# Performance work log

Measured on AMD Instinct MI355X. Metric: run time of the kernel, lower is better.

Reference implementation:

```python
import jax, jax.numpy as jnp
import numpy as np

K = 27  # num_neighs, hardcoded in module
EPS = 1e-5


def knn_idx(x, k):
    # x: (B, N, 3) -> (B, N, k) indices of k nearest neighbors (self included)
    xx = jnp.sum(x * x, axis=-1)                      # (B, N)
    inner = jnp.einsum('bnd,bmd->bnm', x, x)          # (B, N, N)
    d = 2.0 * inner - xx[:, :, None] - xx[:, None, :] # negative sq dist
    return jax.lax.top_k(d, k)[1]


def graph_feature(f, idx):
    # f: (B, N, C), idx: (B, N, k) -> (B, N, k, 2C) = [neigh - center, center]
    neigh = jax.vmap(lambda fb, ib: fb[ib])(f, idx)   # (B, N, k, C)
    center = jnp.broadcast_to(f[:, :, None, :], neigh.shape)
    return jnp.concatenate([neigh - center, center], axis=-1)


def bn_lrelu(y, g, b, axes):
    m = jnp.mean(y, axis=axes, keepdims=True)
    v = jnp.var(y, axis=axes, keepdims=True)
    y = (y - m) * jax.lax.rsqrt(v + EPS) * g + b
    return jnp.where(y >= 0, y, 0.2 * y)


def edge_conv(f, idx, W, g, b):
    # f: (B, N, C) -> (B, N, C_out); 1x1 conv over (B, 2C, N, k) + BN + LeakyReLU + max over k
    h = graph_feature(f, idx)                         # (B, N, k, 2C)
    y = jnp.einsum('bnkc,oc->bnko', h, W)             # (B, N, k, C_out)
    y = bn_lrelu(y, g, b, axes=(0, 1, 2))
    return jnp.max(y, axis=2)                         # (B, N, C_out)


def setup_inputs() -> dict:
    key = jax.random.key(0)
    ks = jax.random.split(key, 8)
    B, N, latent = 2, 2048, 256
    x = jax.random.normal(ks[0], (B, N, 3), dtype=jnp.float32)
    chans = [(6, 96), (192, 192), (384, 384), (768, 768)]
    inp = {'x': x}
    for i, (cin, cout) in enumerate(chans):
        inp[f'W{i}'] = jax.random.normal(ks[1 + i], (cout, cin), dtype=jnp.float32) * np.sqrt(2.0 / cin).astype(np.float32)
        inp[f'g{i}'] = jnp.ones((cout,), dtype=jnp.float32)
        inp[f'b{i}'] = jnp.zeros((cout,), dtype=jnp.float32)
    inp['W4'] = jax.random.normal(ks[5], (latent, 1440), dtype=jnp.float32) * np.sqrt(2.0 / 1440).astype(np.float32)
    inp['g4'] = jnp.ones((latent,), dtype=jnp.float32)
    inp['b4'] = jnp.zeros((latent,), dtype=jnp.float32)
    return inp


def reference(x, W0, g0, b0, W1, g1, b1, W2, g2, b2, W3, g3, b3, W4, g4, b4):
    # x: (B, N, 3)
    idx = knn_idx(x, K)                               # (B, N, K), fixed for all layers (only_true_neighs=True)
    outs = []
    f = x
    for (W, g, b) in ((W0, g0, b0), (W1, g1, b1), (W2, g2, b2), (W3, g3, b3)):
        f = edge_conv(f, idx, W, g, b)
        outs.append(f)
    h = jnp.concatenate(outs, axis=-1)                # (B, N, 1440)
    y = jnp.einsum('bnc,oc->bno', h, W4)              # (B, N, latent)
    feats = bn_lrelu(y, g4, b4, axes=(0, 1))          # features_per_point (B, N, latent)
    global_feat = jnp.max(feats, axis=1)              # (B, latent)
    return global_feat, feats
```

## Files before the change

### kernel.cpp

```cpp
#include <hip/hip_runtime.h>
#include <hip/hip_bf16.h>

#define BATCH 2
#define NPB   2048
#define NPTS  4096
#define KNB   27
#define FCATC 1440
#define CSTRIDE 1696
#define NSLOT 32
#define PBATCH 4

#define WOFF_L1 0
#define WOFF_L2 36864
#define WOFF_L3 184320
#define WOFF_F  774144
#define WTOTAL  1142784

typedef __hip_bfloat16 bf16;
typedef __attribute__((ext_vector_type(8))) short short8;
typedef __attribute__((ext_vector_type(4))) float f32x4;
typedef __attribute__((ext_vector_type(2))) short s16x2;

__device__ __forceinline__ float b2f(bf16 v) { return __bfloat162float(v); }

__device__ __forceinline__ void split_bf16(float v, bf16& h, bf16& l) {
    h = __float2bfloat16(v);
    l = __float2bfloat16(v - b2f(h));
}

__device__ __forceinline__ float ldin(const void* p, size_t i, int f32) {
    return f32 ? ((const float*)p)[i] : b2f(((const bf16*)p)[i]);
}

__global__ void k_init(const void* __restrict__ x, int* __restrict__ flag,
                       float* __restrict__ xf, float* __restrict__ slots) {
    if (blockIdx.x < 424) {
        slots[blockIdx.x * 256 + threadIdx.x] = 0.f;
        return;
    }
    __shared__ int s;
    if (threadIdx.x == 0) s = 0;
    __syncthreads();
    const bf16* xb = (const bf16*)x;
    int local = 0;
    for (int i = threadIdx.x; i < NPTS * 3; i += 256) {
        float v = b2f(xb[i]);
        if (!(fabsf(v) < 1e4f)) local = 1;
    }
    if (local) s = 1;
    __syncthreads();
    int f32 = s;
    if (threadIdx.x == 0) flag[0] = f32;
    for (int i = threadIdx.x; i < NPTS * 3; i += 256) xf[i] = ldin(x, i, f32);
}

__global__ __launch_bounds__(256) void k_knn(const float* __restrict__ x, int* __restrict__ idx) {
    __shared__ uint hist4[4][260];
    __shared__ uint hist[256];
    __shared__ int  tix[NPB];
    __shared__ uint s_phigh;
    __shared__ int  s_rem, s_outcnt, s_tiecnt;

    int bn = blockIdx.x, b = bn >> 11, n = bn & (NPB - 1);
    int tid = threadIdx.x;
    int wv = tid >> 6;
    const float* xb = x + (size_t)b * NPB * 3;
    float cx = xb[n * 3 + 0], cy = xb[n * 3 + 1], cz = xb[n * 3 + 2];
    float cc = cx * cx + cy * cy + cz * cz;

    uint u[8];
    #pragma unroll
    for (int j = 0; j < 8; j++) {
        int m = j * 256 + tid;
        float mx = xb[m * 3 + 0], my = xb[m * 3 + 1], mz = xb[m * 3 + 2];
        float d = 2.f * (cx * mx + cy * my + cz * mz) - cc - (mx * mx + my * my + mz * mz);
        uint s = __float_as_uint(d);
        u[j] = (s & 0x80000000u) ? ~s : (s | 0x80000000u);
    }
    if (tid == 0) { s_phigh = 0; s_rem = KNB; s_outcnt = 0; s_tiecnt = 0; }

    for (int pass = 0; pass < 4; pass++) {
        int shift = 24 - pass * 8;
        hist[tid] = 0;
        for (int i = tid; i < 4 * 260; i += 256) ((uint*)hist4)[i] = 0;
        __syncthreads();
        uint phigh = s_phigh;
        #pragma unroll
        for (int j = 0; j < 8; j++) {
            bool in = (pass == 0) || ((u[j] >> (shift + 8)) == phigh);
            if (in) atomicAdd(&hist4[wv][(u[j] >> shift) & 0xFFu], 1u);
        }
        __syncthreads();
        hist[tid] = hist4[0][tid] + hist4[1][tid] + hist4[2][tid] + hist4[3][tid];
        __syncthreads();
        if (tid < 64) {
            int L = tid;
            uint c0 = hist[L * 4 + 0], c1 = hist[L * 4 + 1], c2 = hist[L * 4 + 2], c3 = hist[L * 4 + 3];
            uint s = c0 + c1 + c2 + c3;
            uint acc = s;
            #pragma unroll
            for (int off = 1; off < 64; off <<= 1) {
                uint t = __shfl_down(acc, off);
                if (L + off < 64) acc += t;
            }
            uint excl = acc - s;
            int rem = s_rem;
            if ((int)excl < rem && (int)acc >= rem) {
                uint cs[4] = { c0, c1, c2, c3 };
                uint cum = excl;
                int bsel = 0; uint hb = 0;
                #pragma unroll
                for (int q = 3; q >= 0; q--) {
                    if ((int)cum < rem && (int)(cum + cs[q]) >= rem && hb == 0u && bsel == 0) {
                        bsel = L * 4 + q; hb = cs[q]; cum += cs[q];
                    } else if (bsel == 0 && hb == 0u) {
                        cum += cs[q];
                    }
                }
                int strictlyAbove = (int)(cum - hb);
                s_rem = rem - strictlyAbove;
                s_phigh = (phigh << 8) | (uint)bsel;
            }
        }
        __syncthreads();
    }

    uint T = s_phigh;
    #pragma unroll
    for (int j = 0; j < 8; j++) {
        int m = j * 256 + tid;
        if (u[j] > T) {
            int p = atomicAdd(&s_outcnt, 1);
            idx[bn * KNB + p] = b * NPB + m;
        } else if (u[j] == T) {
            int p = atomicAdd(&s_tiecnt, 1);
            tix[p] = m;
        }
    }
    __syncthreads();
    int outcnt = s_outcnt, rem = s_rem, tiecnt = s_tiecnt;
    if (tiecnt == rem) {
        if (tid < rem) idx[bn * KNB + outcnt + tid] = b * NPB + tix[tid];
    } else if (tid == 0) {
        for (int t = 0; t < rem; t++) {
            int bi = 0;
            for (int q = 1; q < tiecnt; q++) if (tix[q] < tix[bi]) bi = q;
            idx[bn * KNB + outcnt + t] = b * NPB + tix[bi];
            tix[bi] = 0x7fffffff;
        }
    }
}

__global__ void k_l0(const float* __restrict__ xf, const void* __restrict__ W,
                     const int* __restrict__ flag, bf16* __restrict__ Ub, float* __restrict__ Vf) {
    int i = blockIdx.x * 256 + threadIdx.x;
    if (i >= NPTS * 192) return;
    int bn = i / 192, o = i % 192;
    int f32 = flag[0];
    float x0 = xf[bn * 3 + 0], x1 = xf[bn * 3 + 1], x2 = xf[bn * 3 + 2];
    if (o < 96) {
        float r = x0 * ldin(W, o * 6 + 0, f32) + x1 * ldin(W, o * 6 + 1, f32) + x2 * ldin(W, o * 6 + 2, f32);
        Ub[(size_t)bn * 96 + o] = __float2bfloat16(r);
    } else {
        int oo = o - 96;
        float w0 = ldin(W, oo * 6 + 3, f32) - ldin(W, oo * 6 + 0, f32);
        float w1 = ldin(W, oo * 6 + 4, f32) - ldin(W, oo * 6 + 1, f32);
        float w2 = ldin(W, oo * 6 + 5, f32) - ldin(W, oo * 6 + 2, f32);
        Vf[(size_t)bn * 96 + oo] = x0 * w0 + x1 * w1 + x2 * w2;
    }
}

__global__ void k_wt_all(const void* __restrict__ W1, const void* __restrict__ W2,
                         const void* __restrict__ W3, const void* __restrict__ W4,
                         const int* __restrict__ flag,
                         bf16* __restrict__ Wh, bf16* __restrict__ Wl) {
    int i = blockIdx.x * 256 + threadIdx.x;
    if (i >= WTOTAL) return;
    int f32 = flag[0];
    float w;
    if (i < WOFF_L2) {
        int row = i / 96, c = i % 96;
        w = (row < 192) ? ldin(W1, (size_t)row * 192 + c, f32)
                        : ldin(W1, (size_t)(row - 192) * 192 + 96 + c, f32)
                          - ldin(W1, (size_t)(row - 192) * 192 + c, f32);
    } else if (i < WOFF_L3) {
        int j = i - WOFF_L2;
        int row = j / 192, c = j % 192;
        w = (row < 384) ? ldin(W2, (size_t)row * 384 + c, f32)
                        : ldin(W2, (size_t)(row - 384) * 384 + 192 + c, f32)
                          - ldin(W2, (size_t)(row - 384) * 384 + c, f32);
    } else if (i < WOFF_F) {
        int j = i - WOFF_L3;
        int row = j / 384, c = j % 384;
        w = (row < 768) ? ldin(W3, (size_t)row * 768 + c, f32)
                        : ldin(W3, (size_t)(row - 768) * 768 + 384 + c, f32)
                          - ldin(W3, (size_t)(row - 768) * 768 + c, f32);
    } else {
        int j = i - WOFF_F;
        w = ldin(W4, j, f32);
    }
    bf16 h, l; split_bf16(w, h, l);
    Wh[i] = h; Wl[i] = l;
}

__global__ __launch_bounds__(256) void k_gemm_mfma(const bf16* __restrict__ Ah, const bf16* __restrict__ Al,
                                                   int lda, int aoff,
                                                   const bf16* __restrict__ Bh, const bf16* __restrict__ Bl,
                                                   int K, bf16* __restrict__ Cu, float* __restrict__ Cv,
                                                   int Cosplit, int ldc, int ksz, int zstride) {
    __shared__ bf16 Ash[64][40];
    __shared__ bf16 Asl[64][40];
    __shared__ bf16 Bsh[64][40];
    __shared__ bf16 Bsl[64][40];
    int tid = threadIdx.x;
    int wave = tid >> 6, lane = tid & 63;
    int wm = wave >> 1, wn = wave & 1;
    int quad = lane >> 4, l15 = lane & 15;
    int Lxy = blockIdx.y * gridDim.x + blockIdx.x;
    int stripe = Lxy & 7;
    int w = Lxy >> 3;
    int mb = stripe * 8 + (w & 7);
    int nb = w >> 3;
    int m0 = mb * 64, n0 = nb * 64;
    int kbase = blockIdx.z * ksz;
    float* Cz = Cv + (size_t)blockIdx.z * zstride;
    int lr = tid >> 2, lc = (tid & 3) * 8;

    f32x4 acc[2][2] = {};
    for (int k0 = kbase; k0 < kbase + ksz; k0 += 32) {
        size_t ao = (size_t)(m0 + lr) * lda + aoff + k0 + lc;
        size_t bo = (size_t)(n0 + lr) * K + k0 + lc;
        *(short8*)&Ash[lr][lc] = *(const short8*)&Ah[ao];
        *(short8*)&Asl[lr][lc] = *(const short8*)&Al[ao];
        *(short8*)&Bsh[lr][lc] = *(const short8*)&Bh[bo];
        *(short8*)&Bsl[lr][lc] = *(const short8*)&Bl[bo];
        __syncthreads();
        short8 ah0 = *(const short8*)&Ash[wm * 32 + l15][quad * 8];
        short8 ah1 = *(const short8*)&Ash[wm * 32 + 16 + l15][quad * 8];
        short8 al0 = *(const short8*)&Asl[wm * 32 + l15][quad * 8];
        short8 al1 = *(const short8*)&Asl[wm * 32 + 16 + l15][quad * 8];
        short8 bh0 = *(const short8*)&Bsh[wn * 32 + l15][quad * 8];
        short8 bh1 = *(const short8*)&Bsh[wn * 32 + 16 + l15][quad * 8];
        short8 bl0 = *(const short8*)&Bsl[wn * 32 + l15][quad * 8];
        short8 bl1 = *(const short8*)&Bsl[wn * 32 + 16 + l15][quad * 8];
        acc[0][0] = __builtin_amdgcn_mfma_f32_16x16x32_bf16(ah0, bl0, acc[0][0], 0, 0, 0);
        acc[0][0] = __builtin_amdgcn_mfma_f32_16x16x32_bf16(al0, bh0, acc[0][0], 0, 0, 0);
        acc[0][0] = __builtin_amdgcn_mfma_f32_16x16x32_bf16(ah0, bh0, acc[0][0], 0, 0, 0);
        acc[0][1] = __builtin_amdgcn_mfma_f32_16x16x32_bf16(ah0, bl1, acc[0][1], 0, 0, 0);
        acc[0][1] = __builtin_amdgcn_mfma_f32_16x16x32_bf16(al0, bh1, acc[0][1], 0, 0, 0);
        acc[0][1] = __builtin_amdgcn_mfma_f32_16x16x32_bf16(ah0, bh1, acc[0][1], 0, 0, 0);
        acc[1][0] = __builtin_amdgcn_mfma_f32_16x16x32_bf16(ah1, bl0, acc[1][0], 0, 0, 0);
        acc[1][0] = __builtin_amdgcn_mfma_f32_16x16x32_bf16(al1, bh0, acc[1][0], 0, 0, 0);
        acc[1][0] = __builtin_amdgcn_mfma_f32_16x16x32_bf16(ah1, bh0, acc[1][0], 0, 0, 0);
        acc[1][1] = __builtin_amdgcn_mfma_f32_16x16x32_bf16(ah1, bl1, acc[1][1], 0, 0, 0);
        acc[1][1] = __builtin_amdgcn_mfma_f32_16x16x32_bf16(al1, bh1, acc[1][1], 0, 0, 0);
        acc[1][1] = __builtin_amdgcn_mfma_f32_16x16x32_bf16(ah1, bh1, acc[1][1], 0, 0, 0);
        __syncthreads();
    }
    #pragma unroll
    for (int mt = 0; mt < 2; mt++) {
        #pragma unroll
        for (int nt = 0; nt < 2; nt++) {
            int col = n0 + wn * 32 + nt * 16 + l15;
            #pragma unroll
            for (int i = 0; i < 4; i++) {
                int row = m0 + wm * 32 + mt * 16 + quad * 4 + i;
                if (Cosplit > 0) {
                    if (col < Cosplit) Cu[(size_t)row * Cosplit + col] = __float2bfloat16(acc[mt][nt][i]);
                    else               Cv[(size_t)row * Cosplit + col - Cosplit] = acc[mt][nt][i];
                } else {
                    Cz[(size_t)row * ldc + col] = acc[mt][nt][i];
                }
            }
        }
    }
}

__global__ __launch_bounds__(256) void k_gather(const bf16* __restrict__ Ub, float* __restrict__ Vf,
                                                const int* __restrict__ idx,
                                                bf16* __restrict__ fch, bf16* __restrict__ fcl,
                                                float* __restrict__ ssum, float* __restrict__ ssq,
                                                int Co, int out_off) {
    __shared__ int srow[PBATCH * KNB];
    int tid = threadIdx.x;
    int L = blockIdx.y * gridDim.x + blockIdx.x;
    int batch = L & 1;
    int w = L >> 1;
    int pg = batch * 512 + (w & 511);
    int chunk = w >> 9;
    int p0 = pg * PBATCH;
    if (tid < PBATCH * KNB) srow[tid] = idx[p0 * KNB + tid] * Co;
    __syncthreads();
    int P = Co >> 1;
    int op = chunk * 256 + tid;
    if (op >= P) return;
    int o = op * 2;
    int slot = pg & (NSLOT - 1);
    float s0 = 0.f, s1 = 0.f, q0 = 0.f, q1 = 0.f;
    #pragma unroll 1
    for (int p = 0; p < PBATCH; p++) {
        int bn = p0 + p;
        float2 vv = *(const float2*)&Vf[(size_t)bn * Co + o];
        float ymax0 = -INFINITY, ymax1 = -INFINITY, ymin0 = INFINITY, ymin1 = INFINITY;
        #pragma unroll
        for (int k = 0; k < KNB; k++) {
            uint wb = *(const uint*)&Ub[(size_t)srow[p * KNB + k] + o];
            float y0 = __uint_as_float(wb << 16) + vv.x;
            float y1 = __uint_as_float(wb & 0xffff0000u) + vv.y;
            ymax0 = fmaxf(ymax0, y0); ymin0 = fminf(ymin0, y0); s0 += y0; q0 += y0 * y0;
            ymax1 = fmaxf(ymax1, y1); ymin1 = fminf(ymin1, y1); s1 += y1; q1 += y1 * y1;
        }
        size_t fi = (size_t)bn * FCATC + out_off + o;
        bf16 hh[2], ll[2];
        split_bf16(ymax0, hh[0], ll[0]);
        split_bf16(ymax1, hh[1], ll[1]);
        *(s16x2*)&fch[fi] = *(const s16x2*)hh;
        *(s16x2*)&fcl[fi] = *(const s16x2*)ll;
        *(float2*)&Vf[(size_t)bn * Co + o] = make_float2(ymin0, ymin1);
    }
    atomicAdd(&ssum[slot * CSTRIDE + o + 0], s0);
    atomicAdd(&ssum[slot * CSTRIDE + o + 1], s1);
    atomicAdd(&ssq [slot * CSTRIDE + o + 0], q0);
    atomicAdd(&ssq [slot * CSTRIDE + o + 1], q1);
}

__global__ void k_scaleshift(const float* __restrict__ ssum, const float* __restrict__ ssq,
                             const void* __restrict__ g, const void* __restrict__ bb,
                             const int* __restrict__ flag,
                             float* __restrict__ scale, float* __restrict__ shift, int Co, float invcnt) {
    int o = blockIdx.x * 256 + threadIdx.x;
    if (o >= Co) return;
    int f32 = flag[0];
    float s = 0.f, q = 0.f;
    for (int c = 0; c < NSLOT; c++) { s += ssum[c * CSTRIDE + o]; q += ssq[c * CSTRIDE + o]; }
    float mean = s * invcnt;
    float var = q * invcnt - mean * mean;
    float sc = ldin(g, o, f32) * rsqrtf(var + 1e-5f);
    scale[o] = sc;
    shift[o] = ldin(bb, o, f32) - mean * sc;
}

__global__ __launch_bounds__(256) void k_apply(const float* __restrict__ Vf,
                                               const float* __restrict__ scale, const float* __restrict__ shift,
                                               bf16* __restrict__ fch, bf16* __restrict__ fcl,
                                               int Co, int out_off) {
    int bn = blockIdx.x;
    for (int o = threadIdx.x; o < Co; o += 256) {
        float sc = scale[o], sh = shift[o];
        size_t fi = (size_t)bn * FCATC + out_off + o;
        float y = (sc >= 0.f) ? (b2f(fch[fi]) + b2f(fcl[fi]))
                              : Vf[(size_t)bn * Co + o];
        float z = sc * y + sh;
        z = (z >= 0.f) ? z : 0.2f * z;
        bf16 h, l; split_bf16(z, h, l);
        fch[fi] = h; fcl[fi] = l;
    }
}

__global__ void k_stats_final(const float* __restrict__ part, float* __restrict__ Y,
                              float* __restrict__ ssum, float* __restrict__ ssq) {
    int o = threadIdx.x;
    int p0 = blockIdx.x * 128;
    const size_t PL = (size_t)NPTS * 256;
    float s = 0, q = 0;
    for (int p = 0; p < 128; p++) {
        size_t i = (size_t)(p0 + p) * 256 + o;
        float y = part[i] + part[i + PL] + part[i + 2 * PL] + part[i + 3 * PL] + part[i + 4 * PL];
        Y[i] = y;
        s += y; q += y * y;
    }
    ssum[blockIdx.x * CSTRIDE + o] = s;
    ssq [blockIdx.x * CSTRIDE + o] = q;
}

__global__ void k_feats(const float* __restrict__ Y, const float* __restrict__ ssum,
                        const float* __restrict__ ssq, const void* __restrict__ g,
                        const void* __restrict__ bb, const int* __restrict__ flag,
                        void* __restrict__ out, float* __restrict__ partial) {
    int o = threadIdx.x;
    int chunk = blockIdx.x;
    int bn0 = chunk * 64;
    int f32 = flag[0];
    float s = 0.f, q = 0.f;
    for (int c = 0; c < NSLOT; c++) { s += ssum[c * CSTRIDE + o]; q += ssq[c * CSTRIDE + o]; }
    float mean = s * (1.f / (float)NPTS);
    float var = q * (1.f / (float)NPTS) - mean * mean;
    float sc = ldin(g, o, f32) * rsqrtf(var + 1e-5f);
    float sh = ldin(bb, o, f32) - mean * sc;
    float best = -INFINITY;
    for (int i = 0; i < 64; i++) {
        int bn = bn0 + i;
        float z = sc * Y[(size_t)bn * 256 + o] + sh;
        z = (z >= 0.f) ? z : 0.2f * z;
        size_t oi = (size_t)BATCH * 256 + (size_t)bn * 256 + o;
        if (f32) ((float*)out)[oi] = z;
        else     ((bf16*)out)[oi] = __float2bfloat16(z);
        best = fmaxf(best, z);
    }
    partial[chunk * 256 + o] = best;
}

__global__ void k_gmax(const float* __restrict__ partial, void* __restrict__ out, const int* __restrict__ flag) {
    int o = threadIdx.x;
    int b = blockIdx.x;
    float best = -INFINITY;
    for (int c = 0; c < 32; c++) best = fmaxf(best, partial[(b * 32 + c) * 256 + o]);
    if (flag[0]) ((float*)out)[b * 256 + o] = best;
    else         ((bf16*)out)[b * 256 + o] = __float2bfloat16(best);
}

extern "C" void kernel_launch(void* const* d_in, const int* in_sizes, int n_in,
                              void* d_out, int out_size, void* d_ws, size_t ws_size,
                              hipStream_t stream) {
    const void* x = d_in[0];

    char* ws = (char*)d_ws;
    int*   idx    = (int*)  (ws + 0);
    bf16*  Ub     = (bf16*) (ws + 442368);
    float* Vf     = (float*)(ws + 6733824);
    float* part   = (float*)(ws + 442368);
    bf16*  fch    = (bf16*) (ws + 25608192);
    bf16*  fcl    = (bf16*) (ws + 37404672);
    float* Y4     = (float*)(ws + 49201152);
    bf16*  Whall  = (bf16*) (ws + 53395456);
    bf16*  Wlall  = (bf16*) (ws + 55681024);
    float* slots  = (float*)(ws + 57966592);
    float* ssum   = slots;
    float* ssq    = slots + NSLOT * CSTRIDE;
    float* scales = (float*)(ws + 58400768);
    float* shifts = (float*)(ws + 58407552);
    float* partial= (float*)(ws + 58414336);
    float* xf     = (float*)(ws + 58479872);
    int*   flag   = (int*)  (ws + 58529024);

    const int Cin[4]  = {3, 96, 192, 384};
    const int Co[4]   = {96, 192, 384, 768};
    const int ooff[4] = {0, 96, 288, 672};
    const int soff[5] = {0, 96, 288, 672, 1440};
    const int woff[4] = {0, WOFF_L1, WOFF_L2, WOFF_L3};

    hipLaunchKernelGGL(k_init, dim3(425), dim3(256), 0, stream, x, flag, xf, slots);
    hipLaunchKernelGGL(k_knn, dim3(NPTS), dim3(256), 0, stream, xf, idx);
    hipLaunchKernelGGL(k_wt_all, dim3((WTOTAL + 255) / 256), dim3(256), 0, stream,
                       d_in[4], d_in[7], d_in[10], d_in[13], flag, Whall, Wlall);

    const float invcnt_edge = 1.f / (float)(NPTS * KNB);
    for (int L = 0; L < 4; L++) {
        const void* W  = d_in[1 + 3 * L];
        const void* g  = d_in[2 + 3 * L];
        const void* bb = d_in[3 + 3 * L];
        int N2 = 2 * Co[L];
        if (L == 0) {
            hipLaunchKernelGGL(k_l0, dim3((NPTS * 192 + 255) / 256), dim3(256), 0, stream,
                               xf, W, flag, Ub, Vf);
        } else {
            hipLaunchKernelGGL(k_gemm_mfma, dim3(N2 / 64, NPTS / 64, 1), dim3(256), 0, stream,
                               fch, fcl, FCATC, ooff[L - 1], Whall + woff[L], Wlall + woff[L], Cin[L],
                               Ub, Vf, Co[L], 0, Cin[L], 0);
        }
        int nchunks = ((Co[L] / 2) + 255) / 256;
        hipLaunchKernelGGL(k_gather, dim3(NPTS / PBATCH, nchunks), dim3(256), 0, stream,
                           Ub, Vf, idx, fch, fcl, ssum + soff[L], ssq + soff[L], Co[L], ooff[L]);
        hipLaunchKernelGGL(k_scaleshift, dim3((Co[L] + 255) / 256), dim3(256), 0, stream,
                           ssum + soff[L], ssq + soff[L], g, bb, flag,
                           scales + soff[L], shifts + soff[L], Co[L], invcnt_edge);
        hipLaunchKernelGGL(k_apply, dim3(NPTS), dim3(256), 0, stream,
                           Vf, scales + soff[L], shifts + soff[L], fch, fcl, Co[L], ooff[L]);
    }

    const void* g4 = d_in[14];
    const void* b4 = d_in[15];
    hipLaunchKernelGGL(k_gemm_mfma, dim3(256 / 64, NPTS / 64, 5), dim3(256), 0, stream,
                       fch, fcl, FCATC, 0, Whall + WOFF_F, Wlall + WOFF_F, FCATC,
                       (bf16*)nullptr, part, 0, 256, 288, NPTS * 256);
    hipLaunchKernelGGL(k_stats_final, dim3(32), dim3(256), 0, stream, part, Y4, ssum + soff[4], ssq + soff[4]);
    hipLaunchKernelGGL(k_feats, dim3(64), dim3(256), 0, stream, Y4, ssum + soff[4], ssq + soff[4],
                       g4, b4, flag, d_out, partial);
    hipLaunchKernelGGL(k_gmax, dim3(BATCH), dim3(256), 0, stream, partial, d_out, flag);
}
```

Measured before the change: 343.7 us.

## Fuse BN scale/shift and LeakyReLU into GEMM A-tile loads, drop apply kernels

```diff
diff --git a/kernel.cpp b/kernel.cpp
--- a/kernel.cpp
+++ b/kernel.cpp
@@ -9,6 +9,7 @@
 #define CSTRIDE 1696
 #define NSLOT 32
 #define PBATCH 4
+#define INVCNT_EDGE (1.f / (float)(NPTS * KNB))
 
 #define WOFF_L1 0
 #define WOFF_L2 36864
@@ -22,6 +23,7 @@
 typedef __attribute__((ext_vector_type(2))) short s16x2;
 
 __device__ __forceinline__ float b2f(bf16 v) { return __bfloat162float(v); }
+__device__ __forceinline__ float su2f(short v) { return __uint_as_float(((uint)(unsigned short)v) << 16); }
 
 __device__ __forceinline__ void split_bf16(float v, bf16& h, bf16& l) {
     h = __float2bfloat16(v);
@@ -172,11 +174,30 @@
 
 __global__ void k_wt_all(const void* __restrict__ W1, const void* __restrict__ W2,
                          const void* __restrict__ W3, const void* __restrict__ W4,
+                         const void* __restrict__ g0, const void* __restrict__ b0,
+                         const void* __restrict__ g1, const void* __restrict__ b1,
+                         const void* __restrict__ g2, const void* __restrict__ b2,
+                         const void* __restrict__ g3, const void* __restrict__ b3,
                          const int* __restrict__ flag,
-                         bf16* __restrict__ Wh, bf16* __restrict__ Wl) {
+                         bf16* __restrict__ Wh, bf16* __restrict__ Wl,
+                         float* __restrict__ gall, float* __restrict__ ball) {
     int i = blockIdx.x * 256 + threadIdx.x;
-    if (i >= WTOTAL) return;
+    if (i >= WTOTAL + 2880) return;
     int f32 = flag[0];
+    if (i >= WTOTAL) {
+        int j = i - WTOTAL;
+        int isb = (j >= 1440);
+        int c = isb ? j - 1440 : j;
+        const void* p;
+        int lo;
+        if (c < 96)       { p = isb ? b0 : g0; lo = 0;   }
+        else if (c < 288) { p = isb ? b1 : g1; lo = 96;  }
+        else if (c < 672) { p = isb ? b2 : g2; lo = 288; }
+        else              { p = isb ? b3 : g3; lo = 672; }
+        float v = ldin(p, c - lo, f32);
+        if (isb) ball[c] = v; else gall[c] = v;
+        return;
+    }
     float w;
     if (i < WOFF_L2) {
         int row = i / 96, c = i % 96;
@@ -204,14 +225,18 @@
 }
 
 __global__ __launch_bounds__(256) void k_gemm_mfma(const bf16* __restrict__ Ah, const bf16* __restrict__ Al,
+                                                   const bf16* __restrict__ Amn,
                                                    int lda, int aoff,
                                                    const bf16* __restrict__ Bh, const bf16* __restrict__ Bl,
                                                    int K, bf16* __restrict__ Cu, float* __restrict__ Cv,
-                                                   int Cosplit, int ldc, int ksz, int zstride) {
+                                                   int Cosplit, int ldc, int ksz, int zstride,
+                                                   const float* __restrict__ ssum, const float* __restrict__ ssq,
+                                                   const float* __restrict__ gall, const float* __restrict__ ball) {
     __shared__ bf16 Ash[64][40];
     __shared__ bf16 Asl[64][40];
     __shared__ bf16 Bsh[64][40];
     __shared__ bf16 Bsl[64][40];
+    __shared__ float sls[384], shs[384];
     int tid = threadIdx.x;
     int wave = tid >> 6, lane = tid & 63;
     int wm = wave >> 1, wn = wave & 1;
@@ -226,12 +251,37 @@
     float* Cz = Cv + (size_t)blockIdx.z * zstride;
     int lr = tid >> 2, lc = (tid & 3) * 8;
 
+    for (int k = tid; k < ksz; k += 256) {
+        int c = aoff + kbase + k;
+        float s = 0.f, q = 0.f;
+        for (int c2 = 0; c2 < NSLOT; c2++) { s += ssum[c2 * CSTRIDE + c]; q += ssq[c2 * CSTRIDE + c]; }
+        float mean = s * INVCNT_EDGE;
+        float var = q * INVCNT_EDGE - mean * mean;
+        float sc = gall[c] * rsqrtf(var + 1e-5f);
+        sls[k] = sc;
+        shs[k] = ball[c] - mean * sc;
+    }
+    __syncthreads();
+
     f32x4 acc[2][2] = {};
     for (int k0 = kbase; k0 < kbase + ksz; k0 += 32) {
         size_t ao = (size_t)(m0 + lr) * lda + aoff + k0 + lc;
         size_t bo = (size_t)(n0 + lr) * K + k0 + lc;
-        *(short8*)&Ash[lr][lc] = *(const short8*)&Ah[ao];
-        *(short8*)&Asl[lr][lc] = *(const short8*)&Al[ao];
+        short8 hv = *(const short8*)&Ah[ao];
+        short8 lv = *(const short8*)&Al[ao];
+        short8 mv = *(const short8*)&Amn[ao];
+        bf16 zh[8], zl[8];
+        int kl = k0 - kbase + lc;
+        #pragma unroll
+        for (int j = 0; j < 8; j++) {
+            float sc = sls[kl + j], sh = shs[kl + j];
+            float y = (sc >= 0.f) ? (su2f(hv[j]) + su2f(lv[j])) : su2f(mv[j]);
+            float z = sc * y + sh;
+            z = (z >= 0.f) ? z : 0.2f * z;
+            split_bf16(z, zh[j], zl[j]);
+        }
+        *(short8*)&Ash[lr][lc] = *(const short8*)zh;
+        *(short8*)&Asl[lr][lc] = *(const short8*)zl;
         *(short8*)&Bsh[lr][lc] = *(const short8*)&Bh[bo];
         *(short8*)&Bsl[lr][lc] = *(const short8*)&Bl[bo];
         __syncthreads();
@@ -276,9 +326,10 @@
     }
 }
 
-__global__ __launch_bounds__(256) void k_gather(const bf16* __restrict__ Ub, float* __restrict__ Vf,
+__global__ __launch_bounds__(256) void k_gather(const bf16* __restrict__ Ub, const float* __restrict__ Vf,
                                                 const int* __restrict__ idx,
                                                 bf16* __restrict__ fch, bf16* __restrict__ fcl,
+                                                bf16* __restrict__ fmn,
                                                 float* __restrict__ ssum, float* __restrict__ ssq,
                                                 int Co, int out_off) {
     __shared__ int srow[PBATCH * KNB];
@@ -311,50 +362,19 @@
             ymax1 = fmaxf(ymax1, y1); ymin1 = fminf(ymin1, y1); s1 += y1; q1 += y1 * y1;
         }
         size_t fi = (size_t)bn * FCATC + out_off + o;
-        bf16 hh[2], ll[2];
+        bf16 hh[2], ll[2], mm[2];
         split_bf16(ymax0, hh[0], ll[0]);
         split_bf16(ymax1, hh[1], ll[1]);
+        mm[0] = __float2bfloat16(ymin0);
+        mm[1] = __float2bfloat16(ymin1);
         *(s16x2*)&fch[fi] = *(const s16x2*)hh;
         *(s16x2*)&fcl[fi] = *(const s16x2*)ll;
-        *(float2*)&Vf[(size_t)bn * Co + o] = make_float2(ymin0, ymin1);
+        *(s16x2*)&fmn[fi] = *(const s16x2*)mm;
     }
     atomicAdd(&ssum[slot * CSTRIDE + o + 0], s0);
     atomicAdd(&ssum[slot * CSTRIDE + o + 1], s1);
     atomicAdd(&ssq [slot * CSTRIDE + o + 0], q0);
     atomicAdd(&ssq [slot * CSTRIDE + o + 1], q1);
-}
-
-__global__ void k_scaleshift(const float* __restrict__ ssum, const float* __restrict__ ssq,
-                             const void* __restrict__ g, const void* __restrict__ bb,
-                             const int* __restrict__ flag,
-                             float* __restrict__ scale, float* __restrict__ shift, int Co, float invcnt) {
-    int o = blockIdx.x * 256 + threadIdx.x;
-    if (o >= Co) return;
-    int f32 = flag[0];
-    float s = 0.f, q = 0.f;
-    for (int c = 0; c < NSLOT; c++) { s += ssum[c * CSTRIDE + o]; q += ssq[c * CSTRIDE + o]; }
-    float mean = s * invcnt;
-    float var = q * invcnt - mean * mean;
-    float sc = ldin(g, o, f32) * rsqrtf(var + 1e-5f);
-    scale[o] = sc;
-    shift[o] = ldin(bb, o, f32) - mean * sc;
-}
-
-__global__ __launch_bounds__(256) void k_apply(const float* __restrict__ Vf,
-                                               const float* __restrict__ scale, const float* __restrict__ shift,
-                                               bf16* __restrict__ fch, bf16* __restrict__ fcl,
-                                               int Co, int out_off) {
-    int bn = blockIdx.x;
-    for (int o = threadIdx.x; o < Co; o += 256) {
-        float sc = scale[o], sh = shift[o];
-        size_t fi = (size_t)bn * FCATC + out_off + o;
-        float y = (sc >= 0.f) ? (b2f(fch[fi]) + b2f(fcl[fi]))
-                              : Vf[(size_t)bn * Co + o];
-        float z = sc * y + sh;
-        z = (z >= 0.f) ? z : 0.2f * z;
-        bf16 h, l; split_bf16(z, h, l);
-        fch[fi] = h; fcl[fi] = l;
-    }
 }
 
 __global__ void k_stats_final(const float* __restrict__ part, float* __restrict__ Y,
@@ -427,11 +447,12 @@
     float* slots  = (float*)(ws + 57966592);
     float* ssum   = slots;
     float* ssq    = slots + NSLOT * CSTRIDE;
-    float* scales = (float*)(ws + 58400768);
-    float* shifts = (float*)(ws + 58407552);
     float* partial= (float*)(ws + 58414336);
     float* xf     = (float*)(ws + 58479872);
     int*   flag   = (int*)  (ws + 58529024);
+    bf16*  fmn    = (bf16*) (ws + 58531840);
+    float* gall   = (float*)(ws + 70328320);
+    float* ball   = (float*)(ws + 70334080);
 
     const int Cin[4]  = {3, 96, 192, 384};
     const int Co[4]   = {96, 192, 384, 768};
@@ -441,40 +462,36 @@
 
     hipLaunchKernelGGL(k_init, dim3(425), dim3(256), 0, stream, x, flag, xf, slots);
     hipLaunchKernelGGL(k_knn, dim3(NPTS), dim3(256), 0, stream, xf, idx);
-    hipLaunchKernelGGL(k_wt_all, dim3((WTOTAL + 255) / 256), dim3(256), 0, stream,
-                       d_in[4], d_in[7], d_in[10], d_in[13], flag, Whall, Wlall);
-
-    const float invcnt_edge = 1.f / (float)(NPTS * KNB);
+    hipLaunchKernelGGL(k_wt_all, dim3((WTOTAL + 2880 + 255) / 256), dim3(256), 0, stream,
+                       d_in[4], d_in[7], d_in[10], d_in[13],
+                       d_in[2], d_in[3], d_in[5], d_in[6],
+                       d_in[8], d_in[9], d_in[11], d_in[12],
+                       flag, Whall, Wlall, gall, ball);
+
     for (int L = 0; L < 4; L++) {
-        const void* W  = d_in[1 + 3 * L];
-        const void* g  = d_in[2 + 3 * L];
-        const void* bb = d_in[3 + 3 * L];
         int N2 = 2 * Co[L];
         if (L == 0) {
             hipLaunchKernelGGL(k_l0, dim3((NPTS * 192 + 255) / 256), dim3(256), 0, stream,
-                               xf, W, flag, Ub, Vf);
+                               xf, d_in[1], flag, Ub, Vf);
         } else {
             hipLaunchKernelGGL(k_gemm_mfma, dim3(N2 / 64, NPTS / 64, 1), dim3(256), 0, stream,
-                               fch, fcl, FCATC, ooff[L - 1], Whall + woff[L], Wlall + woff[L], Cin[L],
-                               Ub, Vf, Co[L], 0, Cin[L], 0);
+                               fch, fcl, fmn, FCATC, ooff[L - 1],
+                               Whall + woff[L], Wlall + woff[L], Cin[L],
+                               Ub, Vf, Co[L], 0, Cin[L], 0,
+                               ssum, ssq, gall, ball);
         }
         int nchunks = ((Co[L] / 2) + 255) / 256;
         hipLaunchKernelGGL(k_gather, dim3(NPTS / PBATCH, nchunks), dim3(256), 0, stream,
-                           Ub, Vf, idx, fch, fcl, ssum + soff[L], ssq + soff[L], Co[L], ooff[L]);
-        hipLaunchKernelGGL(k_scaleshift, dim3((Co[L] + 255) / 256), dim3(256), 0, stream,
-                           ssum + soff[L], ssq + soff[L], g, bb, flag,
-                           scales + soff[L], shifts + soff[L], Co[L], invcnt_edge);
-        hipLaunchKernelGGL(k_apply, dim3(NPTS), dim3(256), 0, stream,
-                           Vf, scales + soff[L], shifts + soff[L], fch, fcl, Co[L], ooff[L]);
-    }
-
-    const void* g4 = d_in[14];
-    const void* b4 = d_in[15];
+                           Ub, Vf, idx, fch, fcl, fmn, ssum + soff[L], ssq + soff[L], Co[L], ooff[L]);
+    }
+
     hipLaunchKernelGGL(k_gemm_mfma, dim3(256 / 64, NPTS / 64, 5), dim3(256), 0, stream,
-                       fch, fcl, FCATC, 0, Whall + WOFF_F, Wlall + WOFF_F, FCATC,
-                       (bf16*)nullptr, part, 0, 256, 288, NPTS * 256);
+                       fch, fcl, fmn, FCATC, 0,
+                       Whall + WOFF_F, Wlall + WOFF_F, FCATC,
+                       (bf16*)nullptr, part, 0, 256, 288, NPTS * 256,
+                       ssum, ssq, gall, ball);
     hipLaunchKernelGGL(k_stats_final, dim3(32), dim3(256), 0, stream, part, Y4, ssum + soff[4], ssq + soff[4]);
     hipLaunchKernelGGL(k_feats, dim3(64), dim3(256), 0, stream, Y4, ssum + soff[4], ssq + soff[4],
-                       g4, b4, flag, d_out, partial);
+                       d_in[14], d_in[15], flag, d_out, partial);
     hipLaunchKernelGGL(k_gmax, dim3(BATCH), dim3(256), 0, stream, partial, d_out, flag);
 }
```

Measured after the change: 356.1 us. 1.04x slower.
